# Kernel optimization log

Measured on AMD Instinct MI355X. Metric: run time of the kernel, lower is better.

The kernel has to match this reference:

```python
import jax, jax.numpy as jnp
import numpy as np

N = 100000      # nodes per graph batch
E = 1600000     # edges per graph batch
F_IN = 128
HID = 128
N_GRAPHS = 64


def gcn_conv(x, edge_index, W, b):
    """PyG GCNConv: add self-loops, symmetric deg^-1/2 normalization, scatter-add."""
    n = x.shape[0]
    xw = x @ W                                  # [N, H]
    src, dst = edge_index[0], edge_index[1]
    # degree including self-loop
    deg = jnp.zeros((n,), xw.dtype).at[dst].add(jnp.ones((src.shape[0],), xw.dtype)) + 1.0
    dinv = jax.lax.rsqrt(deg)                   # deg^-1/2
    norm = (dinv[src] * dinv[dst])[:, None]     # [E, 1]
    msg = xw[src] * norm                        # gather + scale
    agg = jnp.zeros_like(xw).at[dst].add(msg)   # scatter-add
    agg = agg + xw * (dinv * dinv)[:, None]     # self-loop contribution
    return agg + b


def global_mean_pool(x, batch, num_graphs):
    sums = jax.ops.segment_sum(x, batch, num_segments=num_graphs)
    cnts = jax.ops.segment_sum(jnp.ones((x.shape[0],), x.dtype), batch, num_segments=num_graphs)
    return sums / jnp.maximum(cnts, 1.0)[:, None]


def setup_inputs() -> dict:
    key = jax.random.key(0)
    ks = jax.random.split(key, 16)
    s = 1.0 / np.sqrt(F_IN)
    sh = 1.0 / np.sqrt(HID)
    return {
        "x_H": jax.random.normal(ks[0], (N, F_IN), jnp.float32),
        "edge_index_H": jax.random.randint(ks[1], (2, E), 0, N, jnp.int64),
        "x_G": jax.random.normal(ks[2], (N, F_IN), jnp.float32),
        "edge_index_G": jax.random.randint(ks[3], (2, E), 0, N, jnp.int64),
        "batch_H": jnp.sort(jax.random.randint(ks[4], (N,), 0, N_GRAPHS, jnp.int64)),
        "batch_G": jnp.sort(jax.random.randint(ks[5], (N,), 0, N_GRAPHS, jnp.int64)),
        # selector params
        "sel_W1": jax.random.uniform(ks[6], (F_IN, HID), jnp.float32, -s, s),
        "sel_b1": jnp.zeros((HID,), jnp.float32),
        "sel_W2": jax.random.uniform(ks[7], (HID, HID), jnp.float32, -sh, sh),
        "sel_b2": jnp.zeros((HID,), jnp.float32),
        "sel_fcw": jax.random.uniform(ks[8], (HID, 1), jnp.float32, -sh, sh),
        "sel_fcb": jnp.zeros((1,), jnp.float32),
        # embedder params (shared between F and G branches)
        "emb_W1": jax.random.uniform(ks[9], (F_IN, HID), jnp.float32, -s, s),
        "emb_b1": jnp.zeros((HID,), jnp.float32),
        "emb_W2": jax.random.uniform(ks[10], (HID, HID), jnp.float32, -sh, sh),
        "emb_b2": jnp.zeros((HID,), jnp.float32),
    }


def reference(x_H, edge_index_H, x_G, edge_index_G, batch_H, batch_G,
              sel_W1, sel_b1, sel_W2, sel_b2, sel_fcw, sel_fcb,
              emb_W1, emb_b1, emb_W2, emb_b2):
    # selector on H
    h = jax.nn.relu(gcn_conv(x_H, edge_index_H, sel_W1, sel_b1))
    h = jax.nn.relu(gcn_conv(h, edge_index_H, sel_W2, sel_b2))
    p = jax.nn.sigmoid(h @ sel_fcw + sel_fcb)          # [N, 1]

    def embed(x, ei, batch):
        z = jax.nn.relu(gcn_conv(x, ei, emb_W1, emb_b1))
        z = jax.nn.relu(gcn_conv(z, ei, emb_W2, emb_b2))
        return global_mean_pool(z, batch, N_GRAPHS)

    h_F = embed(x_H * p, edge_index_H, batch_H)
    h_G = embed(x_G, edge_index_G, batch_G)
    return (h_F, h_G, p)
```

## Files before the change

### kernel.cpp

```cpp
#include <hip/hip_runtime.h>
#include <cstdint>
#include <cstddef>

#define FEAT 128
#define PSL2 32
#define BSHIFT 7
#define CAP 4096

typedef _Float16 h16;
typedef __attribute__((ext_vector_type(8))) _Float16 h16x8;
typedef __attribute__((ext_vector_type(4))) float f32x4;

__global__ __launch_bounds__(256) void k_cvt(const float* __restrict__ X,
    h16* __restrict__ Y, int nv) {
  int i = blockIdx.x * 256 + threadIdx.x;
  if (i < nv) {
    const float* p = X + (size_t)i * 8;
    float4 a = *(const float4*)p, b = *(const float4*)(p + 4);
    h16x8 o;
    o[0] = (h16)a.x; o[1] = (h16)a.y; o[2] = (h16)a.z; o[3] = (h16)a.w;
    o[4] = (h16)b.x; o[5] = (h16)b.y; o[6] = (h16)b.z; o[7] = (h16)b.w;
    *(h16x8*)&Y[(size_t)i * 8] = o;
  }
}

__global__ __launch_bounds__(256) void k_part(const int* __restrict__ ei,
    unsigned int* __restrict__ pair, int* __restrict__ gcur, int E, int nb) {
  __shared__ int cnt[1024];
  __shared__ int base[1024];
  int per = (E + gridDim.x - 1) / gridDim.x;
  int e0 = blockIdx.x * per;
  int e1 = min(e0 + per, E);
  for (int i = threadIdx.x; i < nb; i += 256) cnt[i] = 0;
  __syncthreads();
  for (int e = e0 + threadIdx.x; e < e1; e += 256)
    atomicAdd(&cnt[ei[E + e] >> BSHIFT], 1);
  __syncthreads();
  for (int i = threadIdx.x; i < nb; i += 256) {
    int c = cnt[i];
    base[i] = c ? atomicAdd(&gcur[i], c) : 0;
    cnt[i] = 0;
  }
  __syncthreads();
  for (int e = e0 + threadIdx.x; e < e1; e += 256) {
    int src = ei[e];
    int dst = ei[E + e];
    int b = dst >> BSHIFT;
    int pos = base[b] + atomicAdd(&cnt[b], 1);
    if (pos < CAP) pair[(size_t)b * CAP + pos] = ((unsigned)src << BSHIFT) | (unsigned)(dst & 127);
  }
}

__global__ __launch_bounds__(1024) void k_bscan(const int* __restrict__ cnt,
    int* __restrict__ boffs, int* __restrict__ offs, int nb, int N, int E) {
  __shared__ int wsum[16];
  __shared__ int carry;
  int tid = threadIdx.x;
  int lane = tid & 63;
  int wid = tid >> 6;
  if (tid == 0) carry = 0;
  for (int base = 0; base < nb; base += 1024) {
    __syncthreads();
    int c0 = carry;
    int i = base + tid;
    int v = (i < nb) ? cnt[i] : 0;
    int x = v;
#pragma unroll
    for (int off = 1; off < 64; off <<= 1) {
      int t = __shfl_up(x, off);
      if (lane >= off) x += t;
    }
    if (lane == 63) wsum[wid] = x;
    __syncthreads();
    if (wid == 0) {
      int t = (lane < 16) ? wsum[lane] : 0;
#pragma unroll
      for (int off = 1; off < 16; off <<= 1) {
        int u = __shfl_up(t, off);
        if (lane >= off) t += u;
      }
      if (lane < 16) wsum[lane] = t;
    }
    __syncthreads();
    int wex = (wid == 0) ? 0 : wsum[wid - 1];
    int o = c0 + wex + (x - v);
    if (i < nb) boffs[i] = o;
    int total = wsum[15];
    __syncthreads();
    if (tid == 0) carry = c0 + total;
  }
  __syncthreads();
  if (tid == 0) { boffs[nb] = carry; offs[N] = E; }
}

__global__ __launch_bounds__(256) void k_bucket(const unsigned int* __restrict__ pair,
    const int* __restrict__ bcnt, const int* __restrict__ boffs,
    int* __restrict__ csr, int* __restrict__ offs, float* __restrict__ dinv,
    int N) {
  int b = blockIdx.x;
  int m = min(bcnt[b], CAP);
  __shared__ int cnt[128];
  __shared__ int noff[128];
  __shared__ int w0tot;
  if (threadIdx.x < 128) cnt[threadIdx.x] = 0;
  __syncthreads();
  const unsigned int* p = pair + (size_t)b * CAP;
  for (int i = threadIdx.x; i < m; i += 256)
    atomicAdd(&cnt[p[i] & 127u], 1);
  __syncthreads();
  int v = 0, x = 0;
  int lane = threadIdx.x & 63, w = threadIdx.x >> 6;
  if (threadIdx.x < 128) {
    v = cnt[threadIdx.x];
    x = v;
#pragma unroll
    for (int o = 1; o < 64; o <<= 1) {
      int t = __shfl_up(x, o);
      if (lane >= o) x += t;
    }
    if (threadIdx.x == 63) w0tot = x;
  }
  __syncthreads();
  int cbase = boffs[b];
  if (threadIdx.x < 128) {
    int ex = x - v + ((w == 1) ? w0tot : 0);
    int g = (b << BSHIFT) + threadIdx.x;
    if (g < N) {
      offs[g] = cbase + ex;
      dinv[g] = 1.0f / sqrtf((float)v + 1.0f);
    }
    noff[threadIdx.x] = ex;
    cnt[threadIdx.x] = 0;
  }
  __syncthreads();
  for (int i = threadIdx.x; i < m; i += 256) {
    unsigned pk = p[i];
    int d = pk & 127u;
    int pos = cbase + noff[d] + atomicAdd(&cnt[d], 1);
    csr[pos] = (int)(pk >> BSHIFT);
  }
}

__global__ __launch_bounds__(256) void k_wprep(const float* __restrict__ W,
    h16* __restrict__ WT) {
  int i = blockIdx.x * 256 + threadIdx.x;
  int k = i >> 7, c = i & 127;
  WT[c * FEAT + k] = (h16)W[(size_t)k * FEAT + c];
}

__device__ inline void acc8(f32x4& lo, f32x4& hi, h16x8 v) {
  lo[0] += (float)v[0]; lo[1] += (float)v[1]; lo[2] += (float)v[2]; lo[3] += (float)v[3];
  hi[0] += (float)v[4]; hi[1] += (float)v[5]; hi[2] += (float)v[6]; hi[3] += (float)v[7];
}

__device__ inline void gather_row8(const h16* __restrict__ XW,
    const int* __restrict__ offs, const int* __restrict__ csr,
    int node, int f0, f32x4& olo, f32x4& ohi) {
  f32x4 lo0 = {0,0,0,0}, hi0 = {0,0,0,0};
  f32x4 lo1 = {0,0,0,0}, hi1 = {0,0,0,0};
  f32x4 lo2 = {0,0,0,0}, hi2 = {0,0,0,0};
  f32x4 lo3 = {0,0,0,0}, hi3 = {0,0,0,0};
  h16x8 sv = *(const h16x8*)&XW[(size_t)node * FEAT + f0];
  acc8(lo0, hi0, sv);
  int s = offs[node], e = offs[node + 1];
  int i = s;
  for (; i + 8 <= e; i += 8) {
    int s0 = csr[i + 0], s1 = csr[i + 1], s2 = csr[i + 2], s3 = csr[i + 3];
    int s4 = csr[i + 4], s5 = csr[i + 5], s6 = csr[i + 6], s7 = csr[i + 7];
    h16x8 v0 = *(const h16x8*)&XW[(size_t)s0 * FEAT + f0];
    h16x8 v1 = *(const h16x8*)&XW[(size_t)s1 * FEAT + f0];
    h16x8 v2 = *(const h16x8*)&XW[(size_t)s2 * FEAT + f0];
    h16x8 v3 = *(const h16x8*)&XW[(size_t)s3 * FEAT + f0];
    h16x8 v4 = *(const h16x8*)&XW[(size_t)s4 * FEAT + f0];
    h16x8 v5 = *(const h16x8*)&XW[(size_t)s5 * FEAT + f0];
    h16x8 v6 = *(const h16x8*)&XW[(size_t)s6 * FEAT + f0];
    h16x8 v7 = *(const h16x8*)&XW[(size_t)s7 * FEAT + f0];
    acc8(lo0, hi0, v0); acc8(lo1, hi1, v1);
    acc8(lo2, hi2, v2); acc8(lo3, hi3, v3);
    acc8(lo0, hi0, v4); acc8(lo1, hi1, v5);
    acc8(lo2, hi2, v6); acc8(lo3, hi3, v7);
  }
  if (i + 4 <= e) {
    int s0 = csr[i + 0], s1 = csr[i + 1], s2 = csr[i + 2], s3 = csr[i + 3];
    h16x8 v0 = *(const h16x8*)&XW[(size_t)s0 * FEAT + f0];
    h16x8 v1 = *(const h16x8*)&XW[(size_t)s1 * FEAT + f0];
    h16x8 v2 = *(const h16x8*)&XW[(size_t)s2 * FEAT + f0];
    h16x8 v3 = *(const h16x8*)&XW[(size_t)s3 * FEAT + f0];
    acc8(lo0, hi0, v0); acc8(lo1, hi1, v1);
    acc8(lo2, hi2, v2); acc8(lo3, hi3, v3);
    i += 4;
  }
  for (; i < e; ++i) {
    int s0 = csr[i];
    h16x8 v0 = *(const h16x8*)&XW[(size_t)s0 * FEAT + f0];
    acc8(lo1, hi1, v0);
  }
  lo0[0]+=lo1[0]; lo0[1]+=lo1[1]; lo0[2]+=lo1[2]; lo0[3]+=lo1[3];
  hi0[0]+=hi1[0]; hi0[1]+=hi1[1]; hi0[2]+=hi1[2]; hi0[3]+=hi1[3];
  lo2[0]+=lo3[0]; lo2[1]+=lo3[1]; lo2[2]+=lo3[2]; lo2[3]+=lo3[3];
  hi2[0]+=hi3[0]; hi2[1]+=hi3[1]; hi2[2]+=hi3[2]; hi2[3]+=hi3[3];
  lo0[0]+=lo2[0]; lo0[1]+=lo2[1]; lo0[2]+=lo2[2]; lo0[3]+=lo2[3];
  hi0[0]+=hi2[0]; hi0[1]+=hi2[1]; hi0[2]+=hi2[2]; hi0[3]+=hi2[3];
  olo = lo0; ohi = hi0;
}

__global__ __launch_bounds__(256) void k_agg(const h16* __restrict__ XW,
    const int* __restrict__ offs, const int* __restrict__ csr,
    const float* __restrict__ dinv, const float* __restrict__ bias,
    h16* __restrict__ out, int n) {
  int gid = threadIdx.x >> 4;
  int lane = threadIdx.x & 15;
  int node = blockIdx.x * 16 + gid;
  if (node >= n) return;
  int f0 = lane * 8;
  f32x4 lo, hi;
  gather_row8(XW, offs, csr, node, f0, lo, hi);
  float d = dinv[node];
  float4 b0 = *(const float4*)&bias[f0];
  float4 b1 = *(const float4*)&bias[f0 + 4];
  h16x8 o;
  o[0] = (h16)fmaxf(lo[0] * d + b0.x, 0.f);
  o[1] = (h16)fmaxf(lo[1] * d + b0.y, 0.f);
  o[2] = (h16)fmaxf(lo[2] * d + b0.z, 0.f);
  o[3] = (h16)fmaxf(lo[3] * d + b0.w, 0.f);
  o[4] = (h16)fmaxf(hi[0] * d + b1.x, 0.f);
  o[5] = (h16)fmaxf(hi[1] * d + b1.y, 0.f);
  o[6] = (h16)fmaxf(hi[2] * d + b1.z, 0.f);
  o[7] = (h16)fmaxf(hi[3] * d + b1.w, 0.f);
  *(h16x8*)&out[(size_t)node * FEAT + f0] = o;
}

__global__ __launch_bounds__(256) void k_agg_pvec(const h16* __restrict__ XW,
    const int* __restrict__ offs, const int* __restrict__ csr,
    const float* __restrict__ dinv, const float* __restrict__ bias,
    const float* __restrict__ fcw, const float* __restrict__ fcb,
    float* __restrict__ p, int n) {
  int gid = threadIdx.x >> 4;
  int lane = threadIdx.x & 15;
  int node = blockIdx.x * 16 + gid;
  if (node >= n) return;
  int f0 = lane * 8;
  f32x4 lo, hi;
  gather_row8(XW, offs, csr, node, f0, lo, hi);
  float d = dinv[node];
  float4 b0 = *(const float4*)&bias[f0];
  float4 b1 = *(const float4*)&bias[f0 + 4];
  float4 w0 = *(const float4*)&fcw[f0];
  float4 w1 = *(const float4*)&fcw[f0 + 4];
  float acc = fmaxf(lo[0] * d + b0.x, 0.f) * w0.x
            + fmaxf(lo[1] * d + b0.y, 0.f) * w0.y
            + fmaxf(lo[2] * d + b0.z, 0.f) * w0.z
            + fmaxf(lo[3] * d + b0.w, 0.f) * w0.w
            + fmaxf(hi[0] * d + b1.x, 0.f) * w1.x
            + fmaxf(hi[1] * d + b1.y, 0.f) * w1.y
            + fmaxf(hi[2] * d + b1.z, 0.f) * w1.z
            + fmaxf(hi[3] * d + b1.w, 0.f) * w1.w;
#pragma unroll
  for (int off = 8; off > 0; off >>= 1) acc += __shfl_xor(acc, off, 16);
  if (lane == 0) p[node] = 1.0f / (1.0f + expf(-(acc + fcb[0])));
}

__global__ __launch_bounds__(256) void k_agg_pool(const h16* __restrict__ XW,
    const int* __restrict__ offs, const int* __restrict__ csr,
    const float* __restrict__ dinv, const float* __restrict__ bias,
    const int* __restrict__ batch, float* __restrict__ part, int n) {
  int g = blockIdx.x / PSL2;
  int s = blockIdx.x % PSL2;
  int lo_ = 0, hi_ = n;
  while (lo_ < hi_) { int m = (lo_ + hi_) >> 1; if (batch[m] < g) lo_ = m + 1; else hi_ = m; }
  int start = lo_;
  hi_ = n;
  while (lo_ < hi_) { int m = (lo_ + hi_) >> 1; if (batch[m] <= g) lo_ = m + 1; else hi_ = m; }
  int end = lo_;
  int len = end - start;
  int per = (len + PSL2 - 1) / PSL2;
  int r0 = start + s * per;
  int r1 = min(r0 + per, end);
  int gid = threadIdx.x >> 4;
  int lane = threadIdx.x & 15;
  int f0 = lane * 8;
  float4 b0 = *(const float4*)&bias[f0];
  float4 b1 = *(const float4*)&bias[f0 + 4];
  f32x4 plo = {0,0,0,0}, phi = {0,0,0,0};
  for (int node = r0 + gid; node < r1; node += 16) {
    f32x4 lo, hi;
    gather_row8(XW, offs, csr, node, f0, lo, hi);
    float d = dinv[node];
    plo[0] += fmaxf(lo[0] * d + b0.x, 0.f);
    plo[1] += fmaxf(lo[1] * d + b0.y, 0.f);
    plo[2] += fmaxf(lo[2] * d + b0.z, 0.f);
    plo[3] += fmaxf(lo[3] * d + b0.w, 0.f);
    phi[0] += fmaxf(hi[0] * d + b1.x, 0.f);
    phi[1] += fmaxf(hi[1] * d + b1.y, 0.f);
    phi[2] += fmaxf(hi[2] * d + b1.z, 0.f);
    phi[3] += fmaxf(hi[3] * d + b1.w, 0.f);
  }
  __shared__ float lds[16 * FEAT];
  *(f32x4*)&lds[gid * FEAT + f0] = plo;
  *(f32x4*)&lds[gid * FEAT + f0 + 4] = phi;
  __syncthreads();
  if (threadIdx.x < FEAT) {
    int f = threadIdx.x;
    float t = 0.f;
#pragma unroll
    for (int q = 0; q < 16; ++q) t += lds[q * FEAT + f];
    part[(size_t)blockIdx.x * FEAT + f] = t;
  }
}

__global__ __launch_bounds__(128) void k_pool_fin(const float* __restrict__ part,
    const int* __restrict__ batch, float* __restrict__ out, int n) {
  int g = blockIdx.x;
  int lo = 0, hi = n;
  while (lo < hi) { int m = (lo + hi) >> 1; if (batch[m] < g) lo = m + 1; else hi = m; }
  int start = lo;
  hi = n;
  while (lo < hi) { int m = (lo + hi) >> 1; if (batch[m] <= g) lo = m + 1; else hi = m; }
  int len = lo - start;
  int f = threadIdx.x;
  float tot = 0.f;
#pragma unroll
  for (int s = 0; s < PSL2; ++s) tot += part[(size_t)(g * PSL2 + s) * FEAT + f];
  out[(size_t)g * FEAT + f] = tot / fmaxf((float)len, 1.0f);
}

__device__ inline h16x8 load8(const float* p) {
  float4 a = *(const float4*)p, b = *(const float4*)(p + 4);
  h16x8 o;
  o[0] = (h16)a.x; o[1] = (h16)a.y; o[2] = (h16)a.z; o[3] = (h16)a.w;
  o[4] = (h16)b.x; o[5] = (h16)b.y; o[6] = (h16)b.z; o[7] = (h16)b.w;
  return o;
}
__device__ inline h16x8 load8(const h16* p) { return *(const h16x8*)p; }

template <typename TI>
__global__ __launch_bounds__(256) void k_gemm_mfma(const TI* __restrict__ X,
    const h16* __restrict__ WT, const float* __restrict__ s1, const float* __restrict__ s2,
    h16* __restrict__ Y, int n) {
  __shared__ __align__(16) h16 lA[128 * FEAT];
  __shared__ __align__(16) h16 lB[128 * FEAT];
  int tid = threadIdx.x;
  int row0 = blockIdx.x * 128;
#pragma unroll
  for (int i = 0; i < 8; ++i) {
    int c = tid + i * 256;
    int r = c >> 4, kc = c & 15;
    int grow = row0 + r;
    h16x8 v;
#pragma unroll
    for (int j = 0; j < 8; ++j) v[j] = (h16)0.f;
    if (grow < n) v = load8(&X[(size_t)grow * FEAT + kc * 8]);
    int byte = r * 256 + ((kc * 16) ^ ((r & 7) << 4));
    *(h16x8*)((char*)lA + byte) = v;
  }
#pragma unroll
  for (int i = 0; i < 8; ++i) {
    int c = tid + i * 256;
    int col = c >> 4, kc = c & 15;
    h16x8 v = *(const h16x8*)&WT[col * FEAT + kc * 8];
    int byte = col * 256 + ((kc * 16) ^ ((col & 7) << 4));
    *(h16x8*)((char*)lB + byte) = v;
  }
  __syncthreads();
  int w = tid >> 6, l = tid & 63;
  int lr = l & 15, lq = l >> 4;
  h16x8 af[2][4];
#pragma unroll
  for (int m = 0; m < 2; ++m)
#pragma unroll
    for (int s = 0; s < 4; ++s) {
      int r = w * 32 + m * 16 + lr;
      int k2 = (s * 32 + lq * 8) * 2;
      int byte = r * 256 + (k2 ^ ((r & 7) << 4));
      af[m][s] = *(const h16x8*)((const char*)lA + byte);
    }
  f32x4 acc[2][8];
#pragma unroll
  for (int m = 0; m < 2; ++m)
#pragma unroll
    for (int nn = 0; nn < 8; ++nn) acc[m][nn] = (f32x4){0.f, 0.f, 0.f, 0.f};
#pragma unroll
  for (int nn = 0; nn < 8; ++nn) {
#pragma unroll
    for (int s = 0; s < 4; ++s) {
      int col = nn * 16 + lr;
      int k2 = (s * 32 + lq * 8) * 2;
      int byte = col * 256 + (k2 ^ ((col & 7) << 4));
      h16x8 bf = *(const h16x8*)((const char*)lB + byte);
      acc[0][nn] = __builtin_amdgcn_mfma_f32_16x16x32_f16(af[0][s], bf, acc[0][nn], 0, 0, 0);
      acc[1][nn] = __builtin_amdgcn_mfma_f32_16x16x32_f16(af[1][s], bf, acc[1][nn], 0, 0, 0);
    }
  }
#pragma unroll
  for (int m = 0; m < 2; ++m) {
#pragma unroll
    for (int r = 0; r < 4; ++r) {
      int grow = row0 + w * 32 + m * 16 + lq * 4 + r;
      if (grow < n) {
        float sc = 1.0f;
        if (s1) sc = s1[grow];
        if (s2) sc *= s2[grow];
#pragma unroll
        for (int nn = 0; nn < 8; ++nn)
          Y[(size_t)grow * FEAT + nn * 16 + lr] = (h16)(acc[m][nn][r] * sc);
      }
    }
  }
}

extern "C" void kernel_launch(void* const* d_in, const int* in_sizes, int n_in,
                              void* d_out, int out_size, void* d_ws, size_t ws_size,
                              hipStream_t stream) {
  const float* x_H    = (const float*)d_in[0];
  const int*   ei_H   = (const int*)d_in[1];
  const float* x_G    = (const float*)d_in[2];
  const int*   ei_G   = (const int*)d_in[3];
  const int*   bat_H  = (const int*)d_in[4];
  const int*   bat_G  = (const int*)d_in[5];
  const float* sel_W1 = (const float*)d_in[6];
  const float* sel_b1 = (const float*)d_in[7];
  const float* sel_W2 = (const float*)d_in[8];
  const float* sel_b2 = (const float*)d_in[9];
  const float* sel_fcw = (const float*)d_in[10];
  const float* sel_fcb = (const float*)d_in[11];
  const float* emb_W1 = (const float*)d_in[12];
  const float* emb_b1 = (const float*)d_in[13];
  const float* emb_W2 = (const float*)d_in[14];
  const float* emb_b2 = (const float*)d_in[15];

  const int N = in_sizes[0] / FEAT;
  const int E = in_sizes[1] / 2;
  const int NG = 64;
  const int NB = (N + 127) >> BSHIFT;

  float* out = (float*)d_out;
  float* hF = out;
  float* hG = out + NG * FEAT;
  float* p  = out + 2 * NG * FEAT;

  char* ws = (char*)d_ws;
  size_t off = 0;
  auto alloc = [&](size_t bytes) -> void* {
    void* ptr = (void*)(ws + off);
    off += (bytes + 511) & ~(size_t)511;
    return ptr;
  };
  const size_t SZH = (size_t)N * FEAT * sizeof(h16);
  const size_t SZP = (size_t)NB * CAP * sizeof(unsigned int);
  const size_t SZB = SZH > SZP ? SZH : SZP;
  h16* A       = (h16*)alloc(SZB);
  h16* B       = (h16*)alloc(SZB);
  h16* C       = (h16*)alloc(SZH);
  h16* x16H    = (h16*)alloc(SZH);
  float* dinvH = (float*)alloc((size_t)N * 4);
  float* dinvG = (float*)alloc((size_t)N * 4);
  int*  offsH  = (int*)alloc((size_t)(N + 1) * 4);
  int*  offsG  = (int*)alloc((size_t)(N + 1) * 4);
  int*  csrH   = (int*)alloc((size_t)E * 4);
  int*  csrG   = (int*)alloc((size_t)E * 4);
  int*  gcurH  = (int*)alloc((size_t)NB * 4);
  int*  gcurG  = (int*)alloc((size_t)NB * 4);
  int*  boffsH = (int*)alloc((size_t)(NB + 1) * 4);
  int*  boffsG = (int*)alloc((size_t)(NB + 1) * 4);
  float* part  = (float*)alloc((size_t)NG * PSL2 * FEAT * 4);
  h16* wtSel1  = (h16*)alloc((size_t)FEAT * FEAT * 2);
  h16* wtSel2  = (h16*)alloc((size_t)FEAT * FEAT * 2);
  h16* wtEmb1  = (h16*)alloc((size_t)FEAT * FEAT * 2);
  h16* wtEmb2  = (h16*)alloc((size_t)FEAT * FEAT * 2);
  (void)ws_size;

  unsigned int* pairH = (unsigned int*)A;
  unsigned int* pairG = (unsigned int*)B;

  const int gGemm = (N + 127) / 128;
  const int gAgg  = (N + 15) / 16;

  k_wprep<<<64, 256, 0, stream>>>(sel_W1, wtSel1);
  k_wprep<<<64, 256, 0, stream>>>(sel_W2, wtSel2);
  k_wprep<<<64, 256, 0, stream>>>(emb_W1, wtEmb1);
  k_wprep<<<64, 256, 0, stream>>>(emb_W2, wtEmb2);
  k_cvt<<<(N * FEAT / 8 + 255) / 256, 256, 0, stream>>>(x_H, x16H, N * FEAT / 8);

  hipMemsetAsync(gcurH, 0, (size_t)NB * 4, stream);
  hipMemsetAsync(gcurG, 0, (size_t)NB * 4, stream);
  k_part<<<256, 256, 0, stream>>>(ei_H, pairH, gcurH, E, NB);
  k_part<<<256, 256, 0, stream>>>(ei_G, pairG, gcurG, E, NB);
  k_bscan<<<1, 1024, 0, stream>>>(gcurH, boffsH, offsH, NB, N, E);
  k_bscan<<<1, 1024, 0, stream>>>(gcurG, boffsG, offsG, NB, N, E);
  k_bucket<<<NB, 256, 0, stream>>>(pairH, gcurH, boffsH, csrH, offsH, dinvH, N);
  k_bucket<<<NB, 256, 0, stream>>>(pairG, gcurG, boffsG, csrG, offsG, dinvG, N);

  k_gemm_mfma<h16><<<gGemm, 256, 0, stream>>>(x16H, wtSel1, dinvH, nullptr, A, N);
  k_agg<<<gAgg, 256, 0, stream>>>(A, offsH, csrH, dinvH, sel_b1, B, N);
  k_gemm_mfma<h16><<<gGemm, 256, 0, stream>>>(B, wtSel2, dinvH, nullptr, C, N);
  k_agg_pvec<<<gAgg, 256, 0, stream>>>(C, offsH, csrH, dinvH, sel_b2, sel_fcw, sel_fcb, p, N);

  k_gemm_mfma<h16><<<gGemm, 256, 0, stream>>>(x16H, wtEmb1, dinvH, p, A, N);
  k_agg<<<gAgg, 256, 0, stream>>>(A, offsH, csrH, dinvH, emb_b1, B, N);
  k_gemm_mfma<h16><<<gGemm, 256, 0, stream>>>(B, wtEmb2, dinvH, nullptr, C, N);
  k_agg_pool<<<NG * PSL2, 256, 0, stream>>>(C, offsH, csrH, dinvH, emb_b2, bat_H, part, N);
  k_pool_fin<<<NG, 128, 0, stream>>>(part, bat_H, hF, N);

  k_gemm_mfma<float><<<gGemm, 256, 0, stream>>>(x_G, wtEmb1, dinvG, nullptr, A, N);
  k_agg<<<gAgg, 256, 0, stream>>>(A, offsG, csrG, dinvG, emb_b1, B, N);
  k_gemm_mfma<h16><<<gGemm, 256, 0, stream>>>(B, wtEmb2, dinvG, nullptr, C, N);
  k_agg_pool<<<NG * PSL2, 256, 0, stream>>>(C, offsG, csrG, dinvG, emb_b2, bat_G, part, N);
  k_pool_fin<<<NG, 128, 0, stream>>>(part, bat_G, hG, N);
}
```

Baseline: 639.3 us.

## Batch F and G embedder branches into one concatenated graph of 2N nodes

Concatenates the H and G graphs into one combined CSR (node and edge offsets applied in bucket build), converts x_G to fp16 up front, and runs the shared embedder GEMM/aggregate/pool kernels once over 2N nodes instead of twice. The aim is to halve launch count for the embedder stages and give larger grids that fill the GPU better. Buffers are reused in place (XC overwritten by the aggregation output), and an extra conversion pass over x_G is added in exchange for removing the fp32-input GEMM path.

```diff
diff --git a/kernel.cpp b/kernel.cpp
--- a/kernel.cpp
+++ b/kernel.cpp
@@ -4,6 +4,7 @@
 
 #define FEAT 128
 #define PSL2 32
+#define NGRAPH 64
 #define BSHIFT 7
 #define CAP 4096
 
@@ -52,7 +53,7 @@
 }
 
 __global__ __launch_bounds__(1024) void k_bscan(const int* __restrict__ cnt,
-    int* __restrict__ boffs, int* __restrict__ offs, int nb, int N, int E) {
+    int* __restrict__ boffs, int* __restrict__ offs, int nb, int tailIdx, int tailVal) {
   __shared__ int wsum[16];
   __shared__ int carry;
   int tid = threadIdx.x;
@@ -90,13 +91,13 @@
     if (tid == 0) carry = c0 + total;
   }
   __syncthreads();
-  if (tid == 0) { boffs[nb] = carry; offs[N] = E; }
+  if (tid == 0) { boffs[nb] = carry; offs[tailIdx] = tailVal; }
 }
 
 __global__ __launch_bounds__(256) void k_bucket(const unsigned int* __restrict__ pair,
     const int* __restrict__ bcnt, const int* __restrict__ boffs,
     int* __restrict__ csr, int* __restrict__ offs, float* __restrict__ dinv,
-    int N) {
+    int N, int nodeOff, int edgeOff) {
   int b = blockIdx.x;
   int m = min(bcnt[b], CAP);
   __shared__ int cnt[128];
@@ -121,13 +122,13 @@
     if (threadIdx.x == 63) w0tot = x;
   }
   __syncthreads();
-  int cbase = boffs[b];
+  int cbase = boffs[b] + edgeOff;
   if (threadIdx.x < 128) {
     int ex = x - v + ((w == 1) ? w0tot : 0);
     int g = (b << BSHIFT) + threadIdx.x;
     if (g < N) {
-      offs[g] = cbase + ex;
-      dinv[g] = 1.0f / sqrtf((float)v + 1.0f);
+      offs[nodeOff + g] = cbase + ex;
+      dinv[nodeOff + g] = 1.0f / sqrtf((float)v + 1.0f);
     }
     noff[threadIdx.x] = ex;
     cnt[threadIdx.x] = 0;
@@ -137,7 +138,7 @@
     unsigned pk = p[i];
     int d = pk & 127u;
     int pos = cbase + noff[d] + atomicAdd(&cnt[d], 1);
-    csr[pos] = (int)(pk >> BSHIFT);
+    csr[pos] = (int)(pk >> BSHIFT) + nodeOff;
   }
 }
 
@@ -263,9 +264,14 @@
 __global__ __launch_bounds__(256) void k_agg_pool(const h16* __restrict__ XW,
     const int* __restrict__ offs, const int* __restrict__ csr,
     const float* __restrict__ dinv, const float* __restrict__ bias,
-    const int* __restrict__ batch, float* __restrict__ part, int n) {
-  int g = blockIdx.x / PSL2;
+    const int* __restrict__ batH, const int* __restrict__ batG,
+    float* __restrict__ part, int n) {
+  int gg = blockIdx.x / PSL2;
   int s = blockIdx.x % PSL2;
+  const int* batch;
+  int nodeBase, g;
+  if (gg < NGRAPH) { batch = batH; nodeBase = 0; g = gg; }
+  else             { batch = batG; nodeBase = n; g = gg - NGRAPH; }
   int lo_ = 0, hi_ = n;
   while (lo_ < hi_) { int m = (lo_ + hi_) >> 1; if (batch[m] < g) lo_ = m + 1; else hi_ = m; }
   int start = lo_;
@@ -283,9 +289,10 @@
   float4 b1 = *(const float4*)&bias[f0 + 4];
   f32x4 plo = {0,0,0,0}, phi = {0,0,0,0};
   for (int node = r0 + gid; node < r1; node += 16) {
+    int row = nodeBase + node;
     f32x4 lo, hi;
-    gather_row8(XW, offs, csr, node, f0, lo, hi);
-    float d = dinv[node];
+    gather_row8(XW, offs, csr, row, f0, lo, hi);
+    float d = dinv[row];
     plo[0] += fmaxf(lo[0] * d + b0.x, 0.f);
     plo[1] += fmaxf(lo[1] * d + b0.y, 0.f);
     plo[2] += fmaxf(lo[2] * d + b0.z, 0.f);
@@ -309,8 +316,14 @@
 }
 
 __global__ __launch_bounds__(128) void k_pool_fin(const float* __restrict__ part,
-    const int* __restrict__ batch, float* __restrict__ out, int n) {
-  int g = blockIdx.x;
+    const int* __restrict__ batH, const int* __restrict__ batG,
+    float* __restrict__ hF, float* __restrict__ hG, int n) {
+  int gg = blockIdx.x;
+  const int* batch;
+  float* outp;
+  int g;
+  if (gg < NGRAPH) { batch = batH; g = gg; outp = hF + (size_t)g * FEAT; }
+  else             { batch = batG; g = gg - NGRAPH; outp = hG + (size_t)g * FEAT; }
   int lo = 0, hi = n;
   while (lo < hi) { int m = (lo + hi) >> 1; if (batch[m] < g) lo = m + 1; else hi = m; }
   int start = lo;
@@ -320,22 +333,15 @@
   int f = threadIdx.x;
   float tot = 0.f;
 #pragma unroll
-  for (int s = 0; s < PSL2; ++s) tot += part[(size_t)(g * PSL2 + s) * FEAT + f];
-  out[(size_t)g * FEAT + f] = tot / fmaxf((float)len, 1.0f);
-}
-
-__device__ inline h16x8 load8(const float* p) {
-  float4 a = *(const float4*)p, b = *(const float4*)(p + 4);
-  h16x8 o;
-  o[0] = (h16)a.x; o[1] = (h16)a.y; o[2] = (h16)a.z; o[3] = (h16)a.w;
-  o[4] = (h16)b.x; o[5] = (h16)b.y; o[6] = (h16)b.z; o[7] = (h16)b.w;
-  return o;
-}
+  for (int s = 0; s < PSL2; ++s) tot += part[(size_t)(gg * PSL2 + s) * FEAT + f];
+  outp[f] = tot / fmaxf((float)len, 1.0f);
+}
+
 __device__ inline h16x8 load8(const h16* p) { return *(const h16x8*)p; }
 
-template <typename TI>
-__global__ __launch_bounds__(256) void k_gemm_mfma(const TI* __restrict__ X,
-    const h16* __restrict__ WT, const float* __restrict__ s1, const float* __restrict__ s2,
+__global__ __launch_bounds__(256) void k_gemm_mfma(const h16* __restrict__ X,
+    const h16* __restrict__ WT, const float* __restrict__ s1,
+    const float* __restrict__ s2, int s2n,
     h16* __restrict__ Y, int n) {
   __shared__ __align__(16) h16 lA[128 * FEAT];
   __shared__ __align__(16) h16 lB[128 * FEAT];
@@ -399,7 +405,7 @@
       if (grow < n) {
         float sc = 1.0f;
         if (s1) sc = s1[grow];
-        if (s2) sc *= s2[grow];
+        if (s2 && grow < s2n) sc *= s2[grow];
 #pragma unroll
         for (int nn = 0; nn < 8; ++nn)
           Y[(size_t)grow * FEAT + nn * 16 + lr] = (h16)(acc[m][nn][r] * sc);
@@ -430,13 +436,13 @@
 
   const int N = in_sizes[0] / FEAT;
   const int E = in_sizes[1] / 2;
-  const int NG = 64;
+  const int N2 = 2 * N;
   const int NB = (N + 127) >> BSHIFT;
 
   float* out = (float*)d_out;
   float* hF = out;
-  float* hG = out + NG * FEAT;
-  float* p  = out + 2 * NG * FEAT;
+  float* hG = out + NGRAPH * FEAT;
+  float* p  = out + 2 * NGRAPH * FEAT;
 
   char* ws = (char*)d_ws;
   size_t off = 0;
@@ -445,24 +451,17 @@
     off += (bytes + 511) & ~(size_t)511;
     return ptr;
   };
-  const size_t SZH = (size_t)N * FEAT * sizeof(h16);
-  const size_t SZP = (size_t)NB * CAP * sizeof(unsigned int);
-  const size_t SZB = SZH > SZP ? SZH : SZP;
-  h16* A       = (h16*)alloc(SZB);
-  h16* B       = (h16*)alloc(SZB);
-  h16* C       = (h16*)alloc(SZH);
-  h16* x16H    = (h16*)alloc(SZH);
-  float* dinvH = (float*)alloc((size_t)N * 4);
-  float* dinvG = (float*)alloc((size_t)N * 4);
-  int*  offsH  = (int*)alloc((size_t)(N + 1) * 4);
-  int*  offsG  = (int*)alloc((size_t)(N + 1) * 4);
-  int*  csrH   = (int*)alloc((size_t)E * 4);
-  int*  csrG   = (int*)alloc((size_t)E * 4);
+  const size_t SZ2 = (size_t)N2 * FEAT * sizeof(h16);
+  h16* XC      = (h16*)alloc(SZ2);
+  h16* A       = (h16*)alloc(SZ2);
+  float* dinvC = (float*)alloc((size_t)N2 * 4);
+  int*  offsC  = (int*)alloc((size_t)(N2 + 1) * 4);
+  int*  csrC   = (int*)alloc((size_t)2 * E * 4);
   int*  gcurH  = (int*)alloc((size_t)NB * 4);
   int*  gcurG  = (int*)alloc((size_t)NB * 4);
   int*  boffsH = (int*)alloc((size_t)(NB + 1) * 4);
   int*  boffsG = (int*)alloc((size_t)(NB + 1) * 4);
-  float* part  = (float*)alloc((size_t)NG * PSL2 * FEAT * 4);
+  float* part  = (float*)alloc((size_t)2 * NGRAPH * PSL2 * FEAT * 4);
   h16* wtSel1  = (h16*)alloc((size_t)FEAT * FEAT * 2);
   h16* wtSel2  = (h16*)alloc((size_t)FEAT * FEAT * 2);
   h16* wtEmb1  = (h16*)alloc((size_t)FEAT * FEAT * 2);
@@ -470,40 +469,40 @@
   (void)ws_size;
 
   unsigned int* pairH = (unsigned int*)A;
-  unsigned int* pairG = (unsigned int*)B;
-
-  const int gGemm = (N + 127) / 128;
-  const int gAgg  = (N + 15) / 16;
+  unsigned int* pairG = (unsigned int*)((char*)A + ((size_t)NB * CAP * 4 + 511 & ~(size_t)511));
+
+  h16* A_lo = A;
+  h16* A_hi = A + (size_t)N * FEAT;
+
+  const int gGemmN  = (N + 127) / 128;
+  const int gGemm2N = (N2 + 127) / 128;
+  const int gAggN   = (N + 15) / 16;
+  const int gAgg2N  = (N2 + 15) / 16;
 
   k_wprep<<<64, 256, 0, stream>>>(sel_W1, wtSel1);
   k_wprep<<<64, 256, 0, stream>>>(sel_W2, wtSel2);
   k_wprep<<<64, 256, 0, stream>>>(emb_W1, wtEmb1);
   k_wprep<<<64, 256, 0, stream>>>(emb_W2, wtEmb2);
-  k_cvt<<<(N * FEAT / 8 + 255) / 256, 256, 0, stream>>>(x_H, x16H, N * FEAT / 8);
+  k_cvt<<<(N * FEAT / 8 + 255) / 256, 256, 0, stream>>>(x_H, XC, N * FEAT / 8);
+  k_cvt<<<(N * FEAT / 8 + 255) / 256, 256, 0, stream>>>(x_G, XC + (size_t)N * FEAT, N * FEAT / 8);
 
   hipMemsetAsync(gcurH, 0, (size_t)NB * 4, stream);
   hipMemsetAsync(gcurG, 0, (size_t)NB * 4, stream);
   k_part<<<256, 256, 0, stream>>>(ei_H, pairH, gcurH, E, NB);
   k_part<<<256, 256, 0, stream>>>(ei_G, pairG, gcurG, E, NB);
-  k_bscan<<<1, 1024, 0, stream>>>(gcurH, boffsH, offsH, NB, N, E);
-  k_bscan<<<1, 1024, 0, stream>>>(gcurG, boffsG, offsG, NB, N, E);
-  k_bucket<<<NB, 256, 0, stream>>>(pairH, gcurH, boffsH, csrH, offsH, dinvH, N);
-  k_bucket<<<NB, 256, 0, stream>>>(pairG, gcurG, boffsG, csrG, offsG, dinvG, N);
-
-  k_gemm_mfma<h16><<<gGemm, 256, 0, stream>>>(x16H, wtSel1, dinvH, nullptr, A, N);
-  k_agg<<<gAgg, 256, 0, stream>>>(A, offsH, csrH, dinvH, sel_b1, B, N);
-  k_gemm_mfma<h16><<<gGemm, 256, 0, stream>>>(B, wtSel2, dinvH, nullptr, C, N);
-  k_agg_pvec<<<gAgg, 256, 0, stream>>>(C, offsH, csrH, dinvH, sel_b2, sel_fcw, sel_fcb, p, N);
-
-  k_gemm_mfma<h16><<<gGemm, 256, 0, stream>>>(x16H, wtEmb1, dinvH, p, A, N);
-  k_agg<<<gAgg, 256, 0, stream>>>(A, offsH, csrH, dinvH, emb_b1, B, N);
-  k_gemm_mfma<h16><<<gGemm, 256, 0, stream>>>(B, wtEmb2, dinvH, nullptr, C, N);
-  k_agg_pool<<<NG * PSL2, 256, 0, stream>>>(C, offsH, csrH, dinvH, emb_b2, bat_H, part, N);
-  k_pool_fin<<<NG, 128, 0, stream>>>(part, bat_H, hF, N);
-
-  k_gemm_mfma<float><<<gGemm, 256, 0, stream>>>(x_G, wtEmb1, dinvG, nullptr, A, N);
-  k_agg<<<gAgg, 256, 0, stream>>>(A, offsG, csrG, dinvG, emb_b1, B, N);
-  k_gemm_mfma<h16><<<gGemm, 256, 0, stream>>>(B, wtEmb2, dinvG, nullptr, C, N);
-  k_agg_pool<<<NG * PSL2, 256, 0, stream>>>(C, offsG, csrG, dinvG, emb_b2, bat_G, part, N);
-  k_pool_fin<<<NG, 128, 0, stream>>>(part, bat_G, hG, N);
-}
+  k_bscan<<<1, 1024, 0, stream>>>(gcurH, boffsH, offsC, NB, N, E);
+  k_bscan<<<1, 1024, 0, stream>>>(gcurG, boffsG, offsC, NB, N2, 2 * E);
+  k_bucket<<<NB, 256, 0, stream>>>(pairH, gcurH, boffsH, csrC, offsC, dinvC, N, 0, 0);
+  k_bucket<<<NB, 256, 0, stream>>>(pairG, gcurG, boffsG, csrC, offsC, dinvC, N, N, E);
+
+  k_gemm_mfma<<<gGemmN, 256, 0, stream>>>(XC, wtSel1, dinvC, nullptr, 0, A_lo, N);
+  k_agg<<<gAggN, 256, 0, stream>>>(A_lo, offsC, csrC, dinvC, sel_b1, A_hi, N);
+  k_gemm_mfma<<<gGemmN, 256, 0, stream>>>(A_hi, wtSel2, dinvC, nullptr, 0, A_lo, N);
+  k_agg_pvec<<<gAggN, 256, 0, stream>>>(A_lo, offsC, csrC, dinvC, sel_b2, sel_fcw, sel_fcb, p, N);
+
+  k_gemm_mfma<<<gGemm2N, 256, 0, stream>>>(XC, wtEmb1, dinvC, p, N, A, N2);
+  k_agg<<<gAgg2N, 256, 0, stream>>>(A, offsC, csrC, dinvC, emb_b1, XC, N2);
+  k_gemm_mfma<<<gGemm2N, 256, 0, stream>>>(XC, wtEmb2, dinvC, nullptr, 0, A, N2);
+  k_agg_pool<<<2 * NGRAPH * PSL2, 256, 0, stream>>>(A, offsC, csrC, dinvC, emb_b2, bat_H, bat_G, part, N);
+  k_pool_fin<<<2 * NGRAPH, 128, 0, stream>>>(part, bat_H, bat_G, hF, hG, N);
+}
```

After: 615.2 us. 3.8% less time.
